# Performance work log

Measured on AMD Instinct MI355X. Metric: run time of the kernel, lower is better.

## Reference

```python
import jax, jax.numpy as jnp
import numpy as np

B, T, H, O = 128, 256, 512, 256  # batch, max_seq, hidden_length, output_token_length
X = O + H  # GRU cell input size (concat of y and attention context)


def _glorot(key, shape):
    fan_in, fan_out = shape[0], shape[1]
    limit = np.sqrt(6.0 / (fan_in + fan_out))
    return jax.random.uniform(key, shape, jnp.float32, -limit, limit)


def setup_inputs() -> dict:
    key = jax.random.key(0)
    ks = jax.random.split(key, 16)
    return {
        "h": jax.random.normal(ks[0], (B, T, H), jnp.float32),
        "s0": jax.random.normal(ks[1], (B, H), jnp.float32),
        # y_dense: Dense(H,tanh) -> Dense(H,tanh) -> Dense(O,linear)
        "Wy1": _glorot(ks[2], (H, H)), "by1": jnp.zeros((H,), jnp.float32),
        "Wy2": _glorot(ks[3], (H, H)), "by2": jnp.zeros((H,), jnp.float32),
        "Wy3": _glorot(ks[4], (H, O)), "by3": jnp.zeros((O,), jnp.float32),
        # e_dense: Dense(H,tanh) on concat([h_i, s]) (2H) -> Dense(1,linear)
        "We1": _glorot(ks[5], (2 * H, H)), "be1": jnp.zeros((H,), jnp.float32),
        "We2": _glorot(ks[6], (H, 1)), "be2": jnp.zeros((1,), jnp.float32),
        # GRU cell weights
        "Wxr": _glorot(ks[7], (X, H)), "Whr": _glorot(ks[8], (H, H)), "br": jnp.zeros((H,), jnp.float32),
        "Wxu": _glorot(ks[9], (X, H)), "Whu": _glorot(ks[10], (H, H)), "bu": jnp.zeros((H,), jnp.float32),
        "Wxh": _glorot(ks[11], (X, H)), "Whh": _glorot(ks[12], (H, H)),
    }


def reference(h, s0, Wy1, by1, Wy2, by2, Wy3, by3, We1, be1, We2, be2,
              Wxr, Whr, br, Wxu, Whu, bu, Wxh, Whh):
    We1_h, We1_s = We1[:H], We1[H:]
    # Precompute encoder-side attention projection once: [B, T, H]
    h_proj = jnp.einsum('bth,hk->btk', h, We1_h)

    def step(s, _):
        # output head (uses state BEFORE update, matching original)
        y = jnp.tanh(s @ Wy1 + by1)
        y = jnp.tanh(y @ Wy2 + by2)
        y = y @ Wy3 + by3  # [B, O]
        # Bahdanau attention over all T encoder positions (vectorized)
        s_proj = s @ We1_s + be1  # [B, H]
        e = jnp.squeeze(jnp.tanh(h_proj + s_proj[:, None, :]) @ We2, -1) + be2[0]  # [B, T]
        a = jax.nn.softmax(e, axis=-1)
        c = jnp.einsum('bt,bth->bh', a, h)  # [B, H]
        # GRU cell on concat([y, c])
        x = jnp.concatenate([y, c], axis=-1)  # [B, O+H]
        r = jax.nn.sigmoid(x @ Wxr + s @ Whr + br)
        u = jax.nn.sigmoid(x @ Wxu + s @ Whu + bu)
        h_cand = jnp.tanh(x @ Wxh + (r * s) @ Whh)
        s_new = (1.0 - u) * h_cand + u * s
        return s_new, y

    _, ys = jax.lax.scan(step, s0, None, length=T)  # ys: [T, B, O]
    return jnp.transpose(ys, (1, 0, 2))  # [B, T, O]
```

## Files before the change

### kernel.cpp

```cpp
#include <hip/hip_runtime.h>

#define B_ 128
#define T_ 256
#define H_ 512
#define O_ 256
#define X_ 768

typedef unsigned short u16;
typedef unsigned int u32;

#if __has_builtin(__builtin_amdgcn_exp2f)
#define EXP2(x) __builtin_amdgcn_exp2f(x)
#else
#define EXP2(x) exp2f(x)
#endif
#if __has_builtin(__builtin_amdgcn_rcpf)
#define RCPF(x) __builtin_amdgcn_rcpf(x)
#else
#define RCPF(x) (1.0f / (x))
#endif

#define LOG2E_F 1.4426950408889634f
#define TWOLOG2E_F 2.8853900817779268f

typedef __attribute__((ext_vector_type(8))) short short8;
typedef __attribute__((ext_vector_type(4))) float f32x4;

__device__ __forceinline__ float bf2f(u16 v) {
  union { u32 u; float f; } c; c.u = ((u32)v) << 16; return c.f;
}
__device__ __forceinline__ u16 f2bf(float f) {
  union { float f; u32 u; } c; c.f = f;
  return (u16)((c.u + 0x7FFFu + ((c.u >> 16) & 1u)) >> 16);
}
__device__ __forceinline__ float ftanh(float x) {
  x = fminf(fmaxf(x, -40.f), 40.f);
  float z = EXP2(x * TWOLOG2E_F);
  return (z - 1.0f) * RCPF(z + 1.0f);
}
__device__ __forceinline__ float fsigm(float x) {
  x = fminf(fmaxf(x, -40.f), 40.f);
  return RCPF(1.0f + EXP2(-x * LOG2E_F));
}

__device__ u16 g_hp[(size_t)B_ * T_ * H_];
__device__ u16 g_hb[(size_t)B_ * T_ * H_];
__device__ float g_s[B_ * H_];
__device__ float g_u[B_ * H_];
__device__ float g_sp[B_ * H_];
__device__ float g_p[B_ * H_];

__device__ float g_wcru[512 * 1024];
__device__ float g_wch[512 * 512];
__device__ float g_bru[1024];
__device__ float g_bh[512];

__device__ u16 g_ah[(size_t)8 * 96 * 512];
__device__ u16 g_al[(size_t)8 * 96 * 512];

__device__ u16 Wy1p[(size_t)32 * 16 * 512];
__device__ u16 Wy2p[(size_t)32 * 16 * 512];
__device__ u16 Wy3p[(size_t)16 * 16 * 512];
__device__ u16 We1sp[(size_t)32 * 16 * 512];
__device__ u16 WRUp[(size_t)64 * 64 * 512];
__device__ u16 WPp[(size_t)32 * 48 * 512];
__device__ u16 Whhp[(size_t)32 * 16 * 512];

__device__ u16 cby1[H_];
__device__ u16 cby2[H_];
__device__ u16 cby3[O_];
__device__ u16 cbe1[H_];
__device__ u16 cWe2[H_];

__device__ __forceinline__ void store_packed(int b, int col, float v) {
  u16 hi = f2bf(v);
  size_t idx = (((size_t)(b >> 4) * 96 + (col >> 5)) << 9) +
               ((((col >> 3) & 3) * 16 + (b & 15)) << 3) + (col & 7);
  g_ah[idx] = hi;
  g_al[idx] = f2bf(v - bf2f(hi));
}

#define DEF_CONV(NAME, ARR, N)                                     \
  __global__ void conv_##NAME(const float* __restrict__ s) {       \
    int i = blockIdx.x * 256 + threadIdx.x;                        \
    if (i < (N)) ARR[i] = f2bf(s[i]);                              \
  }

DEF_CONV(by1, cby1, H_)
DEF_CONV(by2, cby2, H_)
DEF_CONV(by3, cby3, O_)
DEF_CONV(be1, cbe1, H_)
DEF_CONV(We2, cWe2, H_)

__global__ void conv_h(const float* __restrict__ s) {
  size_t i = (size_t)blockIdx.x * 256 + threadIdx.x;
  g_hb[i] = f2bf(s[i]);
}

template <int MODE>
__global__ void __launch_bounds__(256) fgemm_comp(const float* __restrict__ A,
                                                  const float* __restrict__ B) {
  float* C = (MODE == 0) ? g_wcru : (MODE == 1) ? (g_wcru + 512) : g_wch;
  const int ldc = (MODE == 2) ? 512 : 1024;
  __shared__ float Ast[32][72];
  __shared__ float Bs[32][72];
  const int tid = threadIdx.x;
  const int tx = tid & 15, ty = tid >> 4;
  const int n0 = blockIdx.x << 6;
  const int m0 = blockIdx.y << 6;
  float acc[4][4] = {};
  for (int k0 = 0; k0 < 256; k0 += 32) {
    {
      int row = tid >> 2, kq = (tid & 3) << 3;
      const float* src = A + (size_t)(m0 + row) * 256 + k0 + kq;
      float4 v0 = *(const float4*)src;
      float4 v1 = *(const float4*)(src + 4);
      Ast[kq + 0][row] = v0.x; Ast[kq + 1][row] = v0.y;
      Ast[kq + 2][row] = v0.z; Ast[kq + 3][row] = v0.w;
      Ast[kq + 4][row] = v1.x; Ast[kq + 5][row] = v1.y;
      Ast[kq + 6][row] = v1.z; Ast[kq + 7][row] = v1.w;
    }
    {
      int kr = tid >> 3, nq = (tid & 7) << 3;
      const float* src = B + (size_t)(k0 + kr) * 512 + n0 + nq;
      float4 v0 = *(const float4*)src;
      float4 v1 = *(const float4*)(src + 4);
      float* d = &Bs[kr][nq];
      d[0] = v0.x; d[1] = v0.y; d[2] = v0.z; d[3] = v0.w;
      d[4] = v1.x; d[5] = v1.y; d[6] = v1.z; d[7] = v1.w;
    }
    __syncthreads();
#pragma unroll
    for (int kk = 0; kk < 32; ++kk) {
      const float4 a4 = *(const float4*)&Ast[kk][ty << 2];
      const float4 b4 = *(const float4*)&Bs[kk][tx << 2];
      float av[4] = {a4.x, a4.y, a4.z, a4.w};
      float bv[4] = {b4.x, b4.y, b4.z, b4.w};
#pragma unroll
      for (int i = 0; i < 4; ++i)
#pragma unroll
        for (int j = 0; j < 4; ++j) acc[i][j] = fmaf(av[i], bv[j], acc[i][j]);
    }
    __syncthreads();
  }
#pragma unroll
  for (int i = 0; i < 4; ++i)
#pragma unroll
    for (int j = 0; j < 4; ++j)
      C[(size_t)(m0 + ty * 4 + i) * ldc + n0 + tx * 4 + j] = acc[i][j];
}

__global__ void bias_fold(const float* __restrict__ by3,
                          const float* __restrict__ Wxr,
                          const float* __restrict__ Wxu,
                          const float* __restrict__ br,
                          const float* __restrict__ bu,
                          const float* __restrict__ Wxh) {
  int n = blockIdx.x * 256 + threadIdx.x;
  if (n < 1024) {
    const float* W = (n < 512) ? Wxr : Wxu;
    int nn = n & 511;
    float acc = (n < 512) ? br[nn] : bu[nn];
    for (int k = 0; k < 256; ++k) acc += by3[k] * W[(size_t)k * 512 + nn];
    g_bru[n] = acc;
  } else if (n < 1536) {
    int nn = n - 1024;
    float acc = 0.f;
    for (int k = 0; k < 256; ++k) acc += by3[k] * Wxh[(size_t)k * 512 + nn];
    g_bh[nn] = acc;
  }
}

#define DEF_PACKB(NAME, DST, NKT, SRCEXPR)                               \
  __global__ void NAME(const float* __restrict__ S0) {                   \
    int gid = blockIdx.x * 256 + threadIdx.x;                            \
    int l = gid & 63, kt = (gid >> 6) % (NKT);                           \
    int ntile = gid / (64 * (NKT));                                      \
    int n = ntile * 16 + (l & 15);                                       \
    __align__(16) u16 tmp[8];                                            \
    _Pragma("unroll")                                                    \
    for (int j = 0; j < 8; ++j) {                                        \
      int k = kt * 32 + ((l >> 4) << 3) + j;                             \
      tmp[j] = f2bf(SRCEXPR);                                            \
    }                                                                    \
    *(uint4*)(DST + (size_t)gid * 8) = *(const uint4*)tmp;               \
  }

DEF_PACKB(pack_Wy1, Wy1p, 16, S0[(size_t)k * 512 + n])
DEF_PACKB(pack_Wy2, Wy2p, 16, S0[(size_t)k * 512 + n])
DEF_PACKB(pack_Wy3, Wy3p, 16, S0[(size_t)k * 256 + n])
DEF_PACKB(pack_We1s, We1sp, 16, S0[(size_t)(512 + k) * 512 + n])

__global__ void pack_WRU(const float* __restrict__ Wxr, const float* __restrict__ Whr,
                         const float* __restrict__ Wxu, const float* __restrict__ Whu) {
  int gid = blockIdx.x * 256 + threadIdx.x;
  int l = gid & 63, kt = (gid >> 6) & 63;
  int ntile = gid >> 12;
  int n = ntile * 16 + (l & 15);
  int nn = n & 511;
  __align__(16) u16 tmp[8];
#pragma unroll
  for (int j = 0; j < 8; ++j) {
    int k = kt * 32 + ((l >> 4) << 3) + j;
    float v;
    if (k < 512) v = g_wcru[(size_t)k * 1024 + n];
    else if (k < 1024) {
      float x = g_wcru[(size_t)(k - 512) * 1024 + n];
      v = x - bf2f(f2bf(x));
    } else if (k < 1536) {
      v = (n < 512) ? Wxr[(size_t)(k - 1024 + 256) * 512 + nn]
                    : Wxu[(size_t)(k - 1024 + 256) * 512 + nn];
    } else {
      v = (n < 512) ? Whr[(size_t)(k - 1536) * 512 + nn]
                    : Whu[(size_t)(k - 1536) * 512 + nn];
    }
    tmp[j] = f2bf(v);
  }
  *(uint4*)(WRUp + (size_t)gid * 8) = *(const uint4*)tmp;
}

__global__ void pack_WP(const float* __restrict__ Wxh) {
  int gid = blockIdx.x * 256 + threadIdx.x;
  int l = gid & 63, kt = (gid >> 6) % 48;
  int ntile = gid / (64 * 48);
  int n = ntile * 16 + (l & 15);
  __align__(16) u16 tmp[8];
#pragma unroll
  for (int j = 0; j < 8; ++j) {
    int k = kt * 32 + ((l >> 4) << 3) + j;
    float v;
    if (k < 512) v = g_wch[(size_t)k * 512 + n];
    else if (k < 1024) {
      float x = g_wch[(size_t)(k - 512) * 512 + n];
      v = x - bf2f(f2bf(x));
    } else {
      v = Wxh[(size_t)(k - 1024 + 256) * 512 + n];
    }
    tmp[j] = f2bf(v);
  }
  *(uint4*)(WPp + (size_t)gid * 8) = *(const uint4*)tmp;
}

__global__ void pack_Whh(const float* __restrict__ Whh) {
  int gid = blockIdx.x * 256 + threadIdx.x;
  int l = gid & 63, kt = (gid >> 6) & 15;
  int ntile = gid >> 10;
  int n = ntile * 16 + (l & 15);
  __align__(16) u16 tmp[8];
#pragma unroll
  for (int j = 0; j < 8; ++j) {
    int k = kt * 32 + ((l >> 4) << 3) + j;
    tmp[j] = f2bf(Whh[(size_t)k * 512 + n]);
  }
  *(uint4*)(Whhp + (size_t)gid * 8) = *(const uint4*)tmp;
}

__global__ void init_kernel(const float* __restrict__ s0) {
  int g = blockIdx.x * blockDim.x + threadIdx.x;
  if (g < B_ * H_) {
    float v = s0[g];
    g_s[g] = v;
    int b = g >> 9, n = g & 511;
    store_packed(b, 1536 + n, v);
  }
}

__global__ void __launch_bounds__(256) hproj_kernel(const float* __restrict__ hh,
                                                    const float* __restrict__ We1) {
  __shared__ float Ast[32][72];
  __shared__ float Bs[32][72];
  const int tid = threadIdx.x;
  const int tx = tid & 15, ty = tid >> 4;
  const int n0 = blockIdx.x << 6;
  const int m0 = blockIdx.y << 6;
  float acc[4][4] = {};
  for (int k0 = 0; k0 < H_; k0 += 32) {
    {
      int row = tid >> 2, kq = (tid & 3) << 3;
      const float* src = hh + (size_t)(m0 + row) * H_ + k0 + kq;
      float4 v0 = *(const float4*)src;
      float4 v1 = *(const float4*)(src + 4);
      Ast[kq + 0][row] = v0.x; Ast[kq + 1][row] = v0.y;
      Ast[kq + 2][row] = v0.z; Ast[kq + 3][row] = v0.w;
      Ast[kq + 4][row] = v1.x; Ast[kq + 5][row] = v1.y;
      Ast[kq + 6][row] = v1.z; Ast[kq + 7][row] = v1.w;
    }
    {
      int kr = tid >> 3, nq = (tid & 7) << 3;
      const float* src = We1 + (size_t)(k0 + kr) * H_ + n0 + nq;
      float4 v0 = *(const float4*)src;
      float4 v1 = *(const float4*)(src + 4);
      float* d = &Bs[kr][nq];
      d[0] = v0.x; d[1] = v0.y; d[2] = v0.z; d[3] = v0.w;
      d[4] = v1.x; d[5] = v1.y; d[6] = v1.z; d[7] = v1.w;
    }
    __syncthreads();
#pragma unroll
    for (int kk = 0; kk < 32; ++kk) {
      const float4 a4 = *(const float4*)&Ast[kk][ty << 2];
      const float4 b4 = *(const float4*)&Bs[kk][tx << 2];
      float av[4] = {a4.x, a4.y, a4.z, a4.w};
      float bv[4] = {b4.x, b4.y, b4.z, b4.w};
#pragma unroll
      for (int i = 0; i < 4; ++i)
#pragma unroll
        for (int j = 0; j < 4; ++j) acc[i][j] = fmaf(av[i], bv[j], acc[i][j]);
    }
    __syncthreads();
  }
#pragma unroll
  for (int i = 0; i < 4; ++i) {
    u16* dst = g_hp + (size_t)(m0 + ty * 4 + i) * H_ + n0 + tx * 4;
    u32 w0 = (u32)f2bf(acc[i][0]) | ((u32)f2bf(acc[i][1]) << 16);
    u32 w1 = (u32)f2bf(acc[i][2]) | ((u32)f2bf(acc[i][3]) << 16);
    *(u32*)dst = w0;
    *(u32*)(dst + 2) = w1;
  }
}

#define FMA8(pk, sk, A)                                          \
  {                                                              \
    u32 ww0 = pk.x, ww1 = pk.y, ww2 = pk.z, ww3 = pk.w;          \
    A[0] = fmaf(sk, bf2f((u16)(ww0 & 0xffffu)), A[0]);           \
    A[1] = fmaf(sk, bf2f((u16)(ww0 >> 16)), A[1]);               \
    A[2] = fmaf(sk, bf2f((u16)(ww1 & 0xffffu)), A[2]);           \
    A[3] = fmaf(sk, bf2f((u16)(ww1 >> 16)), A[3]);               \
    A[4] = fmaf(sk, bf2f((u16)(ww2 & 0xffffu)), A[4]);           \
    A[5] = fmaf(sk, bf2f((u16)(ww2 >> 16)), A[5]);               \
    A[6] = fmaf(sk, bf2f((u16)(ww3 & 0xffffu)), A[6]);           \
    A[7] = fmaf(sk, bf2f((u16)(ww3 >> 16)), A[7]);               \
  }

template <int KTA0, int NKT_B, int KTW>
__device__ __forceinline__ void gemm_core(const u16* __restrict__ BP, int mt,
                                          int nb, int tid, float* smem) {
  const int l = tid & 63, w = tid >> 6;
  f32x4 acc0 = {0.f, 0.f, 0.f, 0.f}, acc1 = {0.f, 0.f, 0.f, 0.f};
  f32x4 acc2 = {0.f, 0.f, 0.f, 0.f}, acc3 = {0.f, 0.f, 0.f, 0.f};
  const size_t abase = (((size_t)mt * 96 + KTA0 + w * KTW) << 9) + l * 8;
#pragma unroll
  for (int kk = 0; kk < KTW; ++kk) {
    short8 ah = *(const short8*)(g_ah + abase + (size_t)kk * 512);
    short8 al = *(const short8*)(g_al + abase + (size_t)kk * 512);
    const size_t bbase =
        (((size_t)(nb * 4) * NKT_B + w * KTW + kk) << 9) + l * 8;
    short8 b0 = *(const short8*)(BP + bbase);
    short8 b1 = *(const short8*)(BP + bbase + ((size_t)NKT_B << 9));
    short8 b2 = *(const short8*)(BP + bbase + ((size_t)2 * NKT_B << 9));
    short8 b3 = *(const short8*)(BP + bbase + ((size_t)3 * NKT_B << 9));
    acc0 = __builtin_amdgcn_mfma_f32_16x16x32_bf16(ah, b0, acc0, 0, 0, 0);
    acc0 = __builtin_amdgcn_mfma_f32_16x16x32_bf16(al, b0, acc0, 0, 0, 0);
    acc1 = __builtin_amdgcn_mfma_f32_16x16x32_bf16(ah, b1, acc1, 0, 0, 0);
    acc1 = __builtin_amdgcn_mfma_f32_16x16x32_bf16(al, b1, acc1, 0, 0, 0);
    acc2 = __builtin_amdgcn_mfma_f32_16x16x32_bf16(ah, b2, acc2, 0, 0, 0);
    acc2 = __builtin_amdgcn_mfma_f32_16x16x32_bf16(al, b2, acc2, 0, 0, 0);
    acc3 = __builtin_amdgcn_mfma_f32_16x16x32_bf16(ah, b3, acc3, 0, 0, 0);
    acc3 = __builtin_amdgcn_mfma_f32_16x16x32_bf16(al, b3, acc3, 0, 0, 0);
  }
  float* pw = smem + w * 1024;
  const int r0 = (l >> 4) * 4, c0 = l & 15;
#pragma unroll
  for (int r = 0; r < 4; ++r) {
    pw[(r0 + r) * 64 + 0 + c0] = acc0[r];
    pw[(r0 + r) * 64 + 16 + c0] = acc1[r];
    pw[(r0 + r) * 64 + 32 + c0] = acc2[r];
    pw[(r0 + r) * 64 + 48 + c0] = acc3[r];
  }
  __syncthreads();
}

#define EPI_V(row, col)                                              \
  float v = 0.f;                                                     \
  _Pragma("unroll") for (int ww = 0; ww < 8; ++ww)                   \
      v += smem[ww * 1024 + (row) * 64 + (col)];

__global__ void __launch_bounds__(512) k1_y1sp() {
  __shared__ __align__(16) float smem[8192];
  const int tid = threadIdx.x;
  const int bid = blockIdx.x;
  if (bid < 64) {
    const int mt = bid >> 3, nb = bid & 7;
    gemm_core<48, 16, 2>(Wy1p, mt, nb, tid, smem);
#pragma unroll
    for (int rep = 0; rep < 2; ++rep) {
      int idx = rep * 512 + tid, row = idx >> 6, col = idx & 63;
      EPI_V(row, col);
      int gb = mt * 16 + row, gc = nb * 64 + col;
      v += bf2f(cby1[gc]);
      store_packed(gb, 2560 + gc, ftanh(v));
    }
  } else {
    const int blk2 = bid - 64;
    const int mt = blk2 >> 3, nb = blk2 & 7;
    gemm_core<48, 16, 2>(We1sp, mt, nb, tid, smem);
#pragma unroll
    for (int rep = 0; rep < 2; ++rep) {
      int idx = rep * 512 + tid, row = idx >> 6, col = idx & 63;
      EPI_V(row, col);
      int gb = mt * 16 + row, gc = nb * 64 + col;
      g_sp[gb * H_ + gc] = v + bf2f(cbe1[gc]);
    }
  }
}

__global__ void __launch_bounds__(512) k2_y2attn() {
  __shared__ __align__(16) float smem[8192];
  __shared__ float red[16];
  const int tid = threadIdx.x;
  const int bid = blockIdx.x;
  if (bid < 64) {
    const int mt = bid >> 3, nb = bid & 7;
    gemm_core<80, 16, 2>(Wy2p, mt, nb, tid, smem);
#pragma unroll
    for (int rep = 0; rep < 2; ++rep) {
      int idx = rep * 512 + tid, row = idx >> 6, col = idx & 63;
      EPI_V(row, col);
      int gb = mt * 16 + row, gc = nb * 64 + col;
      v += bf2f(cby2[gc]);
      float y2v = ftanh(v);
      store_packed(gb, gc, y2v);
      store_packed(gb, 512 + gc, y2v);
    }
  } else {
    const int b = bid - 64;
    float* sm_e = smem + 1024;
    {
      float spv = g_sp[b * H_ + tid];
      float w2 = bf2f(cWe2[tid]);
      smem[2 * tid] = spv * TWOLOG2E_F;
      smem[2 * tid + 1] = -2.0f * w2;
    }
    __syncthreads();
    const int wv = tid >> 6, l = tid & 63;
    const int rr = l & 15, q = l >> 4;
#pragma unroll
    for (int p = 0; p < 2; ++p) {
      int tp = p * 128 + wv * 16 + rr;
      const u16* rowp = g_hp + ((size_t)(b * T_ + tp) << 9);
      float part = 0.f;
      for (int i = 0; i < 16; ++i) {
        int c0 = i * 32 + q * 8;
        uint4 pk = *(const uint4*)(rowp + c0);
        const float4* swp = reinterpret_cast<const float4*>(smem + 2 * c0);
        float4 f0 = swp[0], f1 = swp[1], f2 = swp[2], f3 = swp[3];
        u32 ww[4] = {pk.x, pk.y, pk.z, pk.w};
        {
          float h0 = bf2f((u16)(ww[0] & 0xffffu)), h1 = bf2f((u16)(ww[0] >> 16));
          float x0 = fmaf(h0, TWOLOG2E_F, f0.x);
          float x1 = fmaf(h1, TWOLOG2E_F, f0.z);
          part = fmaf(f0.y, RCPF(EXP2(x0) + 1.f), part);
          part = fmaf(f0.w, RCPF(EXP2(x1) + 1.f), part);
        }
        {
          float h0 = bf2f((u16)(ww[1] & 0xffffu)), h1 = bf2f((u16)(ww[1] >> 16));
          float x0 = fmaf(h0, TWOLOG2E_F, f1.x);
          float x1 = fmaf(h1, TWOLOG2E_F, f1.z);
          part = fmaf(f1.y, RCPF(EXP2(x0) + 1.f), part);
          part = fmaf(f1.w, RCPF(EXP2(x1) + 1.f), part);
        }
        {
          float h0 = bf2f((u16)(ww[2] & 0xffffu)), h1 = bf2f((u16)(ww[2] >> 16));
          float x0 = fmaf(h0, TWOLOG2E_F, f2.x);
          float x1 = fmaf(h1, TWOLOG2E_F, f2.z);
          part = fmaf(f2.y, RCPF(EXP2(x0) + 1.f), part);
          part = fmaf(f2.w, RCPF(EXP2(x1) + 1.f), part);
        }
        {
          float h0 = bf2f((u16)(ww[3] & 0xffffu)), h1 = bf2f((u16)(ww[3] >> 16));
          float x0 = fmaf(h0, TWOLOG2E_F, f3.x);
          float x1 = fmaf(h1, TWOLOG2E_F, f3.z);
          part = fmaf(f3.y, RCPF(EXP2(x0) + 1.f), part);
          part = fmaf(f3.w, RCPF(EXP2(x1) + 1.f), part);
        }
      }
      part += __shfl_xor(part, 16, 64);
      part += __shfl_xor(part, 32, 64);
      if (q == 0) sm_e[tp] = part;
    }
    __syncthreads();
    float v = (tid < T_) ? sm_e[tid] : -3.0e38f;
    float m = v;
#pragma unroll
    for (int off = 32; off > 0; off >>= 1) m = fmaxf(m, __shfl_xor(m, off, 64));
    if (l == 0) red[wv] = m;
    __syncthreads();
    m = fmaxf(fmaxf(fmaxf(red[0], red[1]), fmaxf(red[2], red[3])),
              fmaxf(fmaxf(red[4], red[5]), fmaxf(red[6], red[7])));
    float pe = (tid < T_) ? EXP2((v - m) * LOG2E_F) : 0.f;
    float ssum = pe;
#pragma unroll
    for (int off = 32; off > 0; off >>= 1) ssum += __shfl_xor(ssum, off, 64);
    if (l == 0) red[8 + wv] = ssum;
    __syncthreads();
    float tot = (red[8] + red[9]) + (red[10] + red[11]) +
                (red[12] + red[13]) + (red[14] + red[15]);
    float ainv = RCPF(tot);
    if (tid < T_) sm_e[tid] = pe * ainv;
    __syncthreads();
    {
      const int ts = tid >> 6, c = tid & 63, n0 = c << 3;
      float a[8] = {};
      for (int tp = ts * 32; tp < ts * 32 + 32; ++tp) {
        uint4 pk = *(const uint4*)(g_hb + ((size_t)(b * T_ + tp) << 9) + n0);
        float av = sm_e[tp];
        FMA8(pk, av, a);
      }
      float* pt = smem + 1536 + ts * 512 + n0;
#pragma unroll
      for (int j = 0; j < 8; ++j) pt[j] = a[j];
    }
    __syncthreads();
    {
      float v2 = 0.f;
#pragma unroll
      for (int kk = 0; kk < 8; ++kk) v2 += smem[1536 + kk * 512 + tid];
      store_packed(b, 1024 + tid, v2);
    }
  }
}

__global__ void __launch_bounds__(512) k3_y3rup(float* __restrict__ out, int t) {
  __shared__ __align__(16) float smem[8192];
  const int tid = threadIdx.x;
  const int bid = blockIdx.x;
  if (bid < 32) {
    const int mt3 = bid >> 2, nb3 = bid & 3;
    gemm_core<0, 16, 2>(Wy3p, mt3, nb3, tid, smem);
#pragma unroll
    for (int rep = 0; rep < 2; ++rep) {
      int idx = rep * 512 + tid, row = idx >> 6, col = idx & 63;
      EPI_V(row, col);
      int gb = mt3 * 16 + row, gc = nb3 * 64 + col;
      v += bf2f(cby3[gc]);
      out[((size_t)gb * T_ + t) * O_ + gc] = v;
    }
  } else if (bid < 160) {
    const int idx2 = bid - 32;
    const int mt = idx2 >> 4, nbz = idx2 & 15;
    gemm_core<0, 64, 8>(WRUp, mt, nbz, tid, smem);
#pragma unroll
    for (int rep = 0; rep < 2; ++rep) {
      int idx = rep * 512 + tid, row = idx >> 6, col = idx & 63;
      EPI_V(row, col);
      int gb = mt * 16 + row, gc = nbz * 64 + col;
      v += g_bru[gc];
      if (gc < 512) {
        float rv = fsigm(v);
        float rs = rv * g_s[gb * H_ + gc];
        store_packed(gb, 2048 + gc, rs);
      } else {
        g_u[gb * H_ + (gc - 512)] = fsigm(v);
      }
    }
  } else {
    const int idx2 = bid - 160;
    const int mt = idx2 >> 3, nb = idx2 & 7;
    gemm_core<0, 48, 6>(WPp, mt, nb, tid, smem);
#pragma unroll
    for (int rep = 0; rep < 2; ++rep) {
      int idx = rep * 512 + tid, row = idx >> 6, col = idx & 63;
      EPI_V(row, col);
      int gb = mt * 16 + row, gc = nb * 64 + col;
      g_p[gb * H_ + gc] = v + g_bh[gc];
    }
  }
}

__global__ void __launch_bounds__(512) k4_hc() {
  __shared__ __align__(16) float smem[8192];
  const int tid = threadIdx.x;
  const int bid = blockIdx.x;
  const int mt = bid >> 3, nb = bid & 7;
  gemm_core<64, 16, 2>(Whhp, mt, nb, tid, smem);
#pragma unroll
  for (int rep = 0; rep < 2; ++rep) {
    int idx = rep * 512 + tid, row = idx >> 6, col = idx & 63;
    EPI_V(row, col);
    int gb = mt * 16 + row, gc = nb * 64 + col;
    int sidx = gb * H_ + gc;
    v += g_p[sidx];
    float hc = ftanh(v);
    float uu = g_u[sidx];
    float sn = (1.f - uu) * hc + uu * g_s[sidx];
    g_s[sidx] = sn;
    store_packed(gb, 1536 + gc, sn);
  }
}

extern "C" void kernel_launch(void* const* d_in, const int* in_sizes, int n_in,
                              void* d_out, int out_size, void* d_ws, size_t ws_size,
                              hipStream_t stream) {
  (void)in_sizes; (void)n_in; (void)out_size; (void)d_ws; (void)ws_size;
  const float* h = (const float*)d_in[0];
  float* out = (float*)d_out;

#define CONV(NAME, IDX, N) \
  hipLaunchKernelGGL(conv_##NAME, dim3(((N) + 255) / 256), dim3(256), 0, stream, \
                     (const float*)d_in[IDX])
  CONV(by1, 3, H_);
  CONV(by2, 5, H_);
  CONV(by3, 7, O_);
  CONV(be1, 9, H_);
  CONV(We2, 10, H_);
#undef CONV
  hipLaunchKernelGGL((fgemm_comp<0>), dim3(8, 8), dim3(256), 0, stream,
                     (const float*)d_in[6], (const float*)d_in[12]);
  hipLaunchKernelGGL((fgemm_comp<1>), dim3(8, 8), dim3(256), 0, stream,
                     (const float*)d_in[6], (const float*)d_in[15]);
  hipLaunchKernelGGL((fgemm_comp<2>), dim3(8, 8), dim3(256), 0, stream,
                     (const float*)d_in[6], (const float*)d_in[18]);
  hipLaunchKernelGGL(bias_fold, dim3(6), dim3(256), 0, stream,
                     (const float*)d_in[7], (const float*)d_in[12],
                     (const float*)d_in[15], (const float*)d_in[14],
                     (const float*)d_in[17], (const float*)d_in[18]);
  hipLaunchKernelGGL(pack_Wy1, dim3(128), dim3(256), 0, stream, (const float*)d_in[2]);
  hipLaunchKernelGGL(pack_Wy2, dim3(128), dim3(256), 0, stream, (const float*)d_in[4]);
  hipLaunchKernelGGL(pack_Wy3, dim3(64), dim3(256), 0, stream, (const float*)d_in[6]);
  hipLaunchKernelGGL(pack_We1s, dim3(128), dim3(256), 0, stream, (const float*)d_in[8]);
  hipLaunchKernelGGL(pack_WRU, dim3(1024), dim3(256), 0, stream,
                     (const float*)d_in[12], (const float*)d_in[13],
                     (const float*)d_in[15], (const float*)d_in[16]);
  hipLaunchKernelGGL(pack_WP, dim3(384), dim3(256), 0, stream,
                     (const float*)d_in[18]);
  hipLaunchKernelGGL(pack_Whh, dim3(128), dim3(256), 0, stream,
                     (const float*)d_in[19]);
  hipLaunchKernelGGL(conv_h, dim3((B_ * T_ * H_) / 256), dim3(256), 0, stream, h);
  hipLaunchKernelGGL(init_kernel, dim3(256), dim3(256), 0, stream,
                     (const float*)d_in[1]);
  hipLaunchKernelGGL(hproj_kernel, dim3(8, 512), dim3(256), 0, stream, h,
                     (const float*)d_in[8]);

  for (int t = 0; t < T_; ++t) {
    hipLaunchKernelGGL(k1_y1sp, dim3(128), dim3(512), 0, stream);
    hipLaunchKernelGGL(k2_y2attn, dim3(192), dim3(512), 0, stream);
    hipLaunchKernelGGL(k3_y3rup, dim3(224), dim3(512), 0, stream, out, t);
    hipLaunchKernelGGL(k4_hc, dim3(64), dim3(512), 0, stream);
  }
}
```

Measured before the change: 9.767 ms.

## Use 32x32 output tiles in step GEMMs and nontemporal loads for encoder reads

Adds a gemm_core32 variant in which each wave computes a 32x32 output tile (two A row tiles times two B column tiles), so every loaded A and B fragment feeds two MFMAs instead of one. Most step GEMMs (y1, We1_s, y2, r/u, and the x projection) switch to this tiling with matching block index and epilogue mappings. The attention loops over h_proj and h now use nontemporal loads to avoid polluting the cache with streamed encoder data. The trade-off is more accumulator registers per wave, and the nontemporal hint may cost reuse if the encoder data would otherwise stay resident in cache across steps.

```diff
diff --git a/kernel.cpp b/kernel.cpp
--- a/kernel.cpp
+++ b/kernel.cpp
@@ -25,6 +25,7 @@
 
 typedef __attribute__((ext_vector_type(8))) short short8;
 typedef __attribute__((ext_vector_type(4))) float f32x4;
+typedef __attribute__((ext_vector_type(4))) unsigned int u32x4;
 
 __device__ __forceinline__ float bf2f(u16 v) {
   union { u32 u; float f; } c; c.u = ((u32)v) << 16; return c.f;
@@ -369,35 +370,74 @@
   __syncthreads();
 }
 
-#define EPI_V(row, col)                                              \
+template <int KTA0, int NKT_B, int KTW>
+__device__ __forceinline__ void gemm_core32(const u16* __restrict__ BP, int mt2,
+                                            int nb2, int tid, float* smem) {
+  const int l = tid & 63, w = tid >> 6;
+  f32x4 a00 = {0.f, 0.f, 0.f, 0.f}, a01 = {0.f, 0.f, 0.f, 0.f};
+  f32x4 a10 = {0.f, 0.f, 0.f, 0.f}, a11 = {0.f, 0.f, 0.f, 0.f};
+  const size_t ab0 = (((size_t)(mt2 * 2) * 96 + KTA0 + w * KTW) << 9) + l * 8;
+  const size_t ab1 = (((size_t)(mt2 * 2 + 1) * 96 + KTA0 + w * KTW) << 9) + l * 8;
+#pragma unroll
+  for (int kk = 0; kk < KTW; ++kk) {
+    short8 ah0 = *(const short8*)(g_ah + ab0 + (size_t)kk * 512);
+    short8 al0 = *(const short8*)(g_al + ab0 + (size_t)kk * 512);
+    short8 ah1 = *(const short8*)(g_ah + ab1 + (size_t)kk * 512);
+    short8 al1 = *(const short8*)(g_al + ab1 + (size_t)kk * 512);
+    const size_t bb0 =
+        (((size_t)(nb2 * 2) * NKT_B + w * KTW + kk) << 9) + l * 8;
+    short8 b0 = *(const short8*)(BP + bb0);
+    short8 b1 = *(const short8*)(BP + bb0 + ((size_t)NKT_B << 9));
+    a00 = __builtin_amdgcn_mfma_f32_16x16x32_bf16(ah0, b0, a00, 0, 0, 0);
+    a00 = __builtin_amdgcn_mfma_f32_16x16x32_bf16(al0, b0, a00, 0, 0, 0);
+    a01 = __builtin_amdgcn_mfma_f32_16x16x32_bf16(ah0, b1, a01, 0, 0, 0);
+    a01 = __builtin_amdgcn_mfma_f32_16x16x32_bf16(al0, b1, a01, 0, 0, 0);
+    a10 = __builtin_amdgcn_mfma_f32_16x16x32_bf16(ah1, b0, a10, 0, 0, 0);
+    a10 = __builtin_amdgcn_mfma_f32_16x16x32_bf16(al1, b0, a10, 0, 0, 0);
+    a11 = __builtin_amdgcn_mfma_f32_16x16x32_bf16(ah1, b1, a11, 0, 0, 0);
+    a11 = __builtin_amdgcn_mfma_f32_16x16x32_bf16(al1, b1, a11, 0, 0, 0);
+  }
+  float* pw = smem + w * 1024;
+  const int r0 = (l >> 4) * 4, c0 = l & 15;
+#pragma unroll
+  for (int r = 0; r < 4; ++r) {
+    pw[(r0 + r) * 32 + c0] = a00[r];
+    pw[(r0 + r) * 32 + 16 + c0] = a01[r];
+    pw[(16 + r0 + r) * 32 + c0] = a10[r];
+    pw[(16 + r0 + r) * 32 + 16 + c0] = a11[r];
+  }
+  __syncthreads();
+}
+
+#define EPI_V(row, col, LD)                                          \
   float v = 0.f;                                                     \
   _Pragma("unroll") for (int ww = 0; ww < 8; ++ww)                   \
-      v += smem[ww * 1024 + (row) * 64 + (col)];
+      v += smem[ww * 1024 + (row) * (LD) + (col)];
 
 __global__ void __launch_bounds__(512) k1_y1sp() {
   __shared__ __align__(16) float smem[8192];
   const int tid = threadIdx.x;
   const int bid = blockIdx.x;
   if (bid < 64) {
-    const int mt = bid >> 3, nb = bid & 7;
-    gemm_core<48, 16, 2>(Wy1p, mt, nb, tid, smem);
+    const int mt2 = bid >> 4, nb2 = bid & 15;
+    gemm_core32<48, 16, 2>(Wy1p, mt2, nb2, tid, smem);
 #pragma unroll
     for (int rep = 0; rep < 2; ++rep) {
-      int idx = rep * 512 + tid, row = idx >> 6, col = idx & 63;
-      EPI_V(row, col);
-      int gb = mt * 16 + row, gc = nb * 64 + col;
+      int idx = rep * 512 + tid, row = idx >> 5, col = idx & 31;
+      EPI_V(row, col, 32);
+      int gb = mt2 * 32 + row, gc = nb2 * 32 + col;
       v += bf2f(cby1[gc]);
       store_packed(gb, 2560 + gc, ftanh(v));
     }
   } else {
     const int blk2 = bid - 64;
-    const int mt = blk2 >> 3, nb = blk2 & 7;
-    gemm_core<48, 16, 2>(We1sp, mt, nb, tid, smem);
+    const int mt2 = blk2 >> 4, nb2 = blk2 & 15;
+    gemm_core32<48, 16, 2>(We1sp, mt2, nb2, tid, smem);
 #pragma unroll
     for (int rep = 0; rep < 2; ++rep) {
-      int idx = rep * 512 + tid, row = idx >> 6, col = idx & 63;
-      EPI_V(row, col);
-      int gb = mt * 16 + row, gc = nb * 64 + col;
+      int idx = rep * 512 + tid, row = idx >> 5, col = idx & 31;
+      EPI_V(row, col, 32);
+      int gb = mt2 * 32 + row, gc = nb2 * 32 + col;
       g_sp[gb * H_ + gc] = v + bf2f(cbe1[gc]);
     }
   }
@@ -409,13 +449,13 @@
   const int tid = threadIdx.x;
   const int bid = blockIdx.x;
   if (bid < 64) {
-    const int mt = bid >> 3, nb = bid & 7;
-    gemm_core<80, 16, 2>(Wy2p, mt, nb, tid, smem);
+    const int mt2 = bid >> 4, nb2 = bid & 15;
+    gemm_core32<80, 16, 2>(Wy2p, mt2, nb2, tid, smem);
 #pragma unroll
     for (int rep = 0; rep < 2; ++rep) {
-      int idx = rep * 512 + tid, row = idx >> 6, col = idx & 63;
-      EPI_V(row, col);
-      int gb = mt * 16 + row, gc = nb * 64 + col;
+      int idx = rep * 512 + tid, row = idx >> 5, col = idx & 31;
+      EPI_V(row, col, 32);
+      int gb = mt2 * 32 + row, gc = nb2 * 32 + col;
       v += bf2f(cby2[gc]);
       float y2v = ftanh(v);
       store_packed(gb, gc, y2v);
@@ -440,7 +480,7 @@
       float part = 0.f;
       for (int i = 0; i < 16; ++i) {
         int c0 = i * 32 + q * 8;
-        uint4 pk = *(const uint4*)(rowp + c0);
+        u32x4 pk = __builtin_nontemporal_load((const u32x4*)(rowp + c0));
         const float4* swp = reinterpret_cast<const float4*>(smem + 2 * c0);
         float4 f0 = swp[0], f1 = swp[1], f2 = swp[2], f3 = swp[3];
         u32 ww[4] = {pk.x, pk.y, pk.z, pk.w};
@@ -501,7 +541,8 @@
       const int ts = tid >> 6, c = tid & 63, n0 = c << 3;
       float a[8] = {};
       for (int tp = ts * 32; tp < ts * 32 + 32; ++tp) {
-        uint4 pk = *(const uint4*)(g_hb + ((size_t)(b * T_ + tp) << 9) + n0);
+        u32x4 pk = __builtin_nontemporal_load(
+            (const u32x4*)(g_hb + ((size_t)(b * T_ + tp) << 9) + n0));
         float av = sm_e[tp];
         FMA8(pk, av, a);
       }
@@ -529,20 +570,20 @@
 #pragma unroll
     for (int rep = 0; rep < 2; ++rep) {
       int idx = rep * 512 + tid, row = idx >> 6, col = idx & 63;
-      EPI_V(row, col);
+      EPI_V(row, col, 64);
       int gb = mt3 * 16 + row, gc = nb3 * 64 + col;
       v += bf2f(cby3[gc]);
       out[((size_t)gb * T_ + t) * O_ + gc] = v;
     }
   } else if (bid < 160) {
     const int idx2 = bid - 32;
-    const int mt = idx2 >> 4, nbz = idx2 & 15;
-    gemm_core<0, 64, 8>(WRUp, mt, nbz, tid, smem);
+    const int mt2 = idx2 >> 5, nb2 = idx2 & 31;
+    gemm_core32<0, 64, 8>(WRUp, mt2, nb2, tid, smem);
 #pragma unroll
     for (int rep = 0; rep < 2; ++rep) {
-      int idx = rep * 512 + tid, row = idx >> 6, col = idx & 63;
-      EPI_V(row, col);
-      int gb = mt * 16 + row, gc = nbz * 64 + col;
+      int idx = rep * 512 + tid, row = idx >> 5, col = idx & 31;
+      EPI_V(row, col, 32);
+      int gb = mt2 * 32 + row, gc = nb2 * 32 + col;
       v += g_bru[gc];
       if (gc < 512) {
         float rv = fsigm(v);
@@ -554,13 +595,13 @@
     }
   } else {
     const int idx2 = bid - 160;
-    const int mt = idx2 >> 3, nb = idx2 & 7;
-    gemm_core<0, 48, 6>(WPp, mt, nb, tid, smem);
+    const int mt2 = idx2 >> 4, nb2 = idx2 & 15;
+    gemm_core32<0, 48, 6>(WPp, mt2, nb2, tid, smem);
 #pragma unroll
     for (int rep = 0; rep < 2; ++rep) {
-      int idx = rep * 512 + tid, row = idx >> 6, col = idx & 63;
-      EPI_V(row, col);
-      int gb = mt * 16 + row, gc = nb * 64 + col;
+      int idx = rep * 512 + tid, row = idx >> 5, col = idx & 31;
+      EPI_V(row, col, 32);
+      int gb = mt2 * 32 + row, gc = nb2 * 32 + col;
       g_p[gb * H_ + gc] = v + g_bh[gc];
     }
   }
@@ -575,7 +616,7 @@
 #pragma unroll
   for (int rep = 0; rep < 2; ++rep) {
     int idx = rep * 512 + tid, row = idx >> 6, col = idx & 63;
-    EPI_V(row, col);
+    EPI_V(row, col, 64);
     int gb = mt * 16 + row, gc = nb * 64 + col;
     int sidx = gb * H_ + gc;
     v += g_p[sidx];
```

Measured after the change: 12.47 ms. +27.7%, slower.

## Halve GEMM output tile width and double attention block threads for more CTAs

Applied to the files above, without the earlier changes.

Adds a 16x32 output-tile MFMA GEMM helper and uses it in the y1/s-proj, y2 and hidden-candidate kernels, doubling their block counts so more of the GPU's compute units are busy per timestep. The attention blocks go to 1024 threads with 16 waves, each wave scoring 16 time positions and the context sum split 16 ways, which shortens the serial work per block. In exchange, reduction and sync overhead rises, and the y2 GEMM now uses 16 waves with one K tile each, giving more partial sums to add.

```diff
diff --git a/kernel.cpp b/kernel.cpp
--- a/kernel.cpp
+++ b/kernel.cpp
@@ -369,62 +369,89 @@
   __syncthreads();
 }
 
-#define EPI_V(row, col)                                              \
+template <int KTA0, int NKT_B, int KTW, int NW>
+__device__ __forceinline__ void gemm_n32(const u16* __restrict__ BP, int mt,
+                                         int nb2, int tid, float* smem) {
+  const int l = tid & 63, w = tid >> 6;
+  f32x4 acc0 = {0.f, 0.f, 0.f, 0.f}, acc1 = {0.f, 0.f, 0.f, 0.f};
+  const size_t abase = (((size_t)mt * 96 + KTA0 + w * KTW) << 9) + l * 8;
+#pragma unroll
+  for (int kk = 0; kk < KTW; ++kk) {
+    short8 ah = *(const short8*)(g_ah + abase + (size_t)kk * 512);
+    short8 al = *(const short8*)(g_al + abase + (size_t)kk * 512);
+    const size_t bbase =
+        (((size_t)(nb2 * 2) * NKT_B + w * KTW + kk) << 9) + l * 8;
+    short8 b0 = *(const short8*)(BP + bbase);
+    short8 b1 = *(const short8*)(BP + bbase + ((size_t)NKT_B << 9));
+    acc0 = __builtin_amdgcn_mfma_f32_16x16x32_bf16(ah, b0, acc0, 0, 0, 0);
+    acc0 = __builtin_amdgcn_mfma_f32_16x16x32_bf16(al, b0, acc0, 0, 0, 0);
+    acc1 = __builtin_amdgcn_mfma_f32_16x16x32_bf16(ah, b1, acc1, 0, 0, 0);
+    acc1 = __builtin_amdgcn_mfma_f32_16x16x32_bf16(al, b1, acc1, 0, 0, 0);
+  }
+  float* pw = smem + w * 512;
+  const int r0 = (l >> 4) * 4, c0 = l & 15;
+#pragma unroll
+  for (int r = 0; r < 4; ++r) {
+    pw[(r0 + r) * 32 + c0] = acc0[r];
+    pw[(r0 + r) * 32 + 16 + c0] = acc1[r];
+  }
+  __syncthreads();
+}
+
+#define EPI_V64(row, col)                                            \
   float v = 0.f;                                                     \
   _Pragma("unroll") for (int ww = 0; ww < 8; ++ww)                   \
       v += smem[ww * 1024 + (row) * 64 + (col)];
 
+#define EPI_V32(row, col, NW)                                        \
+  float v = 0.f;                                                     \
+  _Pragma("unroll") for (int ww = 0; ww < (NW); ++ww)                \
+      v += smem[ww * 512 + (row) * 32 + (col)];
+
 __global__ void __launch_bounds__(512) k1_y1sp() {
-  __shared__ __align__(16) float smem[8192];
+  __shared__ __align__(16) float smem[4096];
   const int tid = threadIdx.x;
   const int bid = blockIdx.x;
-  if (bid < 64) {
-    const int mt = bid >> 3, nb = bid & 7;
-    gemm_core<48, 16, 2>(Wy1p, mt, nb, tid, smem);
-#pragma unroll
-    for (int rep = 0; rep < 2; ++rep) {
-      int idx = rep * 512 + tid, row = idx >> 6, col = idx & 63;
-      EPI_V(row, col);
-      int gb = mt * 16 + row, gc = nb * 64 + col;
-      v += bf2f(cby1[gc]);
-      store_packed(gb, 2560 + gc, ftanh(v));
-    }
+  if (bid < 128) {
+    const int mt = bid >> 4, nb2 = bid & 15;
+    gemm_n32<48, 16, 2, 8>(Wy1p, mt, nb2, tid, smem);
+    int row = tid >> 5, col = tid & 31;
+    EPI_V32(row, col, 8);
+    int gb = mt * 16 + row, gc = nb2 * 32 + col;
+    v += bf2f(cby1[gc]);
+    store_packed(gb, 2560 + gc, ftanh(v));
   } else {
-    const int blk2 = bid - 64;
-    const int mt = blk2 >> 3, nb = blk2 & 7;
-    gemm_core<48, 16, 2>(We1sp, mt, nb, tid, smem);
-#pragma unroll
-    for (int rep = 0; rep < 2; ++rep) {
-      int idx = rep * 512 + tid, row = idx >> 6, col = idx & 63;
-      EPI_V(row, col);
-      int gb = mt * 16 + row, gc = nb * 64 + col;
-      g_sp[gb * H_ + gc] = v + bf2f(cbe1[gc]);
-    }
-  }
-}
-
-__global__ void __launch_bounds__(512) k2_y2attn() {
-  __shared__ __align__(16) float smem[8192];
-  __shared__ float red[16];
+    const int blk2 = bid - 128;
+    const int mt = blk2 >> 4, nb2 = blk2 & 15;
+    gemm_n32<48, 16, 2, 8>(We1sp, mt, nb2, tid, smem);
+    int row = tid >> 5, col = tid & 31;
+    EPI_V32(row, col, 8);
+    int gb = mt * 16 + row, gc = nb2 * 32 + col;
+    g_sp[gb * H_ + gc] = v + bf2f(cbe1[gc]);
+  }
+}
+
+__global__ void __launch_bounds__(1024) k2_y2attn() {
+  __shared__ __align__(16) float smem[10240];
+  __shared__ float red[32];
   const int tid = threadIdx.x;
   const int bid = blockIdx.x;
-  if (bid < 64) {
-    const int mt = bid >> 3, nb = bid & 7;
-    gemm_core<80, 16, 2>(Wy2p, mt, nb, tid, smem);
-#pragma unroll
-    for (int rep = 0; rep < 2; ++rep) {
-      int idx = rep * 512 + tid, row = idx >> 6, col = idx & 63;
-      EPI_V(row, col);
-      int gb = mt * 16 + row, gc = nb * 64 + col;
+  if (bid < 128) {
+    const int mt = bid >> 4, nb2 = bid & 15;
+    gemm_n32<80, 16, 1, 16>(Wy2p, mt, nb2, tid, smem);
+    if (tid < 512) {
+      int row = tid >> 5, col = tid & 31;
+      EPI_V32(row, col, 16);
+      int gb = mt * 16 + row, gc = nb2 * 32 + col;
       v += bf2f(cby2[gc]);
       float y2v = ftanh(v);
       store_packed(gb, gc, y2v);
       store_packed(gb, 512 + gc, y2v);
     }
   } else {
-    const int b = bid - 64;
+    const int b = bid - 128;
     float* sm_e = smem + 1024;
-    {
+    if (tid < 512) {
       float spv = g_sp[b * H_ + tid];
       float w2 = bf2f(cWe2[tid]);
       smem[2 * tid] = spv * TWOLOG2E_F;
@@ -433,9 +460,8 @@
     __syncthreads();
     const int wv = tid >> 6, l = tid & 63;
     const int rr = l & 15, q = l >> 4;
-#pragma unroll
-    for (int p = 0; p < 2; ++p) {
-      int tp = p * 128 + wv * 16 + rr;
+    {
+      int tp = wv * 16 + rr;
       const u16* rowp = g_hp + ((size_t)(b * T_ + tp) << 9);
       float part = 0.f;
       for (int i = 0; i < 16; ++i) {
@@ -484,23 +510,25 @@
     for (int off = 32; off > 0; off >>= 1) m = fmaxf(m, __shfl_xor(m, off, 64));
     if (l == 0) red[wv] = m;
     __syncthreads();
-    m = fmaxf(fmaxf(fmaxf(red[0], red[1]), fmaxf(red[2], red[3])),
-              fmaxf(fmaxf(red[4], red[5]), fmaxf(red[6], red[7])));
+    m = red[0];
+#pragma unroll
+    for (int rI = 1; rI < 16; ++rI) m = fmaxf(m, red[rI]);
     float pe = (tid < T_) ? EXP2((v - m) * LOG2E_F) : 0.f;
     float ssum = pe;
 #pragma unroll
     for (int off = 32; off > 0; off >>= 1) ssum += __shfl_xor(ssum, off, 64);
-    if (l == 0) red[8 + wv] = ssum;
-    __syncthreads();
-    float tot = (red[8] + red[9]) + (red[10] + red[11]) +
-                (red[12] + red[13]) + (red[14] + red[15]);
+    if (l == 0) red[16 + wv] = ssum;
+    __syncthreads();
+    float tot = 0.f;
+#pragma unroll
+    for (int rI = 0; rI < 16; ++rI) tot += red[16 + rI];
     float ainv = RCPF(tot);
     if (tid < T_) sm_e[tid] = pe * ainv;
     __syncthreads();
     {
       const int ts = tid >> 6, c = tid & 63, n0 = c << 3;
       float a[8] = {};
-      for (int tp = ts * 32; tp < ts * 32 + 32; ++tp) {
+      for (int tp = ts * 16; tp < ts * 16 + 16; ++tp) {
         uint4 pk = *(const uint4*)(g_hb + ((size_t)(b * T_ + tp) << 9) + n0);
         float av = sm_e[tp];
         FMA8(pk, av, a);
@@ -510,10 +538,10 @@
       for (int j = 0; j < 8; ++j) pt[j] = a[j];
     }
     __syncthreads();
-    {
+    if (tid < 512) {
       float v2 = 0.f;
 #pragma unroll
-      for (int kk = 0; kk < 8; ++kk) v2 += smem[1536 + kk * 512 + tid];
+      for (int kk = 0; kk < 16; ++kk) v2 += smem[1536 + kk * 512 + tid];
       store_packed(b, 1024 + tid, v2);
     }
   }
@@ -529,7 +557,7 @@
 #pragma unroll
     for (int rep = 0; rep < 2; ++rep) {
       int idx = rep * 512 + tid, row = idx >> 6, col = idx & 63;
-      EPI_V(row, col);
+      EPI_V64(row, col);
       int gb = mt3 * 16 + row, gc = nb3 * 64 + col;
       v += bf2f(cby3[gc]);
       out[((size_t)gb * T_ + t) * O_ + gc] = v;
@@ -541,7 +569,7 @@
 #pragma unroll
     for (int rep = 0; rep < 2; ++rep) {
       int idx = rep * 512 + tid, row = idx >> 6, col = idx & 63;
-      EPI_V(row, col);
+      EPI_V64(row, col);
       int gb = mt * 16 + row, gc = nbz * 64 + col;
       v += g_bru[gc];
       if (gc < 512) {
@@ -559,7 +587,7 @@
 #pragma unroll
     for (int rep = 0; rep < 2; ++rep) {
       int idx = rep * 512 + tid, row = idx >> 6, col = idx & 63;
-      EPI_V(row, col);
+      EPI_V64(row, col);
       int gb = mt * 16 + row, gc = nb * 64 + col;
       g_p[gb * H_ + gc] = v + g_bh[gc];
     }
@@ -567,24 +595,21 @@
 }
 
 __global__ void __launch_bounds__(512) k4_hc() {
-  __shared__ __align__(16) float smem[8192];
+  __shared__ __align__(16) float smem[4096];
   const int tid = threadIdx.x;
   const int bid = blockIdx.x;
-  const int mt = bid >> 3, nb = bid & 7;
-  gemm_core<64, 16, 2>(Whhp, mt, nb, tid, smem);
-#pragma unroll
-  for (int rep = 0; rep < 2; ++rep) {
-    int idx = rep * 512 + tid, row = idx >> 6, col = idx & 63;
-    EPI_V(row, col);
-    int gb = mt * 16 + row, gc = nb * 64 + col;
-    int sidx = gb * H_ + gc;
-    v += g_p[sidx];
-    float hc = ftanh(v);
-    float uu = g_u[sidx];
-    float sn = (1.f - uu) * hc + uu * g_s[sidx];
-    g_s[sidx] = sn;
-    store_packed(gb, 1536 + gc, sn);
-  }
+  const int mt = bid >> 4, nb2 = bid & 15;
+  gemm_n32<64, 16, 2, 8>(Whhp, mt, nb2, tid, smem);
+  int row = tid >> 5, col = tid & 31;
+  EPI_V32(row, col, 8);
+  int gb = mt * 16 + row, gc = nb2 * 32 + col;
+  int sidx = gb * H_ + gc;
+  v += g_p[sidx];
+  float hc = ftanh(v);
+  float uu = g_u[sidx];
+  float sn = (1.f - uu) * hc + uu * g_s[sidx];
+  g_s[sidx] = sn;
+  store_packed(gb, 1536 + gc, sn);
 }
 
 extern "C" void kernel_launch(void* const* d_in, const int* in_sizes, int n_in,
@@ -631,9 +656,9 @@
                      (const float*)d_in[8]);
 
   for (int t = 0; t < T_; ++t) {
-    hipLaunchKernelGGL(k1_y1sp, dim3(128), dim3(512), 0, stream);
-    hipLaunchKernelGGL(k2_y2attn, dim3(192), dim3(512), 0, stream);
+    hipLaunchKernelGGL(k1_y1sp, dim3(256), dim3(512), 0, stream);
+    hipLaunchKernelGGL(k2_y2attn, dim3(256), dim3(1024), 0, stream);
     hipLaunchKernelGGL(k3_y3rup, dim3(224), dim3(512), 0, stream, out, t);
-    hipLaunchKernelGGL(k4_hc, dim3(64), dim3(512), 0, stream);
-  }
-}
+    hipLaunchKernelGGL(k4_hc, dim3(128), dim3(512), 0, stream);
+  }
+}
```

New measurement: 8.648 ms. 11.5% less time.
